# Optimization experiments

Hardware: AMD Instinct MI355X
Metric: run time of the kernel (lower is better)

Reference implementation:

```python
import jax, jax.numpy as jnp
import numpy as np

TAU = 5.0
ENTROPY_REG = 0.0  # entropy branch disabled (matches init kwargs)
NEG_INF = -1.0e9
NORM_EPS = 1e-12   # F.normalize eps
COS_EPS = 1e-8     # F.cosine_similarity eps


def _l2norm(x):
    n = jnp.sqrt(jnp.sum(x * x, axis=-1, keepdims=True))
    return x / jnp.maximum(n, NORM_EPS)


def setup_inputs() -> dict:
    key = jax.random.key(0)
    k1, k2, k3 = jax.random.split(key, 3)
    B, T, D = 8, 2048, 512
    pred_tokens = jax.random.normal(k1, (B, T, D), dtype=jnp.float32)
    text_tokens = jax.random.normal(k2, (B, T, D), dtype=jnp.float32)
    text_pad_mask = jax.random.randint(k3, (B, T), 0, 2).astype(jnp.bool_)  # True = PAD
    return {"pred_tokens": pred_tokens, "text_tokens": text_tokens, "text_pad_mask": text_pad_mask}


def reference(pred_tokens, text_tokens, text_pad_mask):
    B, Tp, D = pred_tokens.shape
    Tt = text_tokens.shape[1]
    T = min(Tp, Tt)
    P = _l2norm(pred_tokens[:, :T, :])            # [B,T,D]
    E = _l2norm(text_tokens[:, :T, :])            # [B,T,D]
    valid = ~text_pad_mask[:, :T]                 # [B,T] True = valid column

    S = jnp.einsum('btd,bsd->bts', P, E)          # [B,T,T]
    S = jnp.where(valid[:, None, :], S, NEG_INF)
    A = jax.nn.softmax(S * TAU, axis=-1)          # [B,T,T]
    E_hat = jnp.einsum('bts,bsd->btd', A, E)      # [B,T,D]

    # cosine similarity with eps-clamped norms (F.cosine_similarity semantics)
    dot = jnp.sum(P * E_hat, axis=-1)             # [B,T]
    pn = jnp.maximum(jnp.sqrt(jnp.sum(P * P, axis=-1)), COS_EPS)
    en = jnp.maximum(jnp.sqrt(jnp.sum(E_hat * E_hat, axis=-1)), COS_EPS)
    cos = dot / (pn * en)                         # [B,T]

    # row_has_valid: per-batch 'any valid column', broadcast over rows
    row_valid = jnp.broadcast_to(jnp.any(valid, axis=-1, keepdims=True), cos.shape)
    w = row_valid.astype(cos.dtype)
    cnt = jnp.sum(w)
    loss_sel = jnp.sum(w * (1.0 - cos)) / jnp.maximum(cnt, 1.0)
    loss = jnp.where(cnt > 0, loss_sel, jnp.zeros((), cos.dtype))
    tas = jnp.where(cnt > 0, 1.0 - jax.lax.stop_gradient(loss), loss)
    return (loss, tas)
```

## Files before the change

kernel.cpp:

```cpp
#include <hip/hip_runtime.h>
#include <cstdint>

typedef float f32x4 __attribute__((ext_vector_type(4)));
typedef long longx2 __attribute__((ext_vector_type(2)));
typedef unsigned char u8;
typedef unsigned short u16;
typedef unsigned int u32;
typedef unsigned long long u64;

#define B_N 8
#define T_N 2048
#define D_N 512
#define TAU 5.0f
#define NROW (B_N * T_N)
#define K1E 7.213475204444817f
#define K2E 1.4426950408889634f

#define WAITV(n) asm volatile("s_waitcnt vmcnt(" #n ")" ::: "memory")
#define BAR      __builtin_amdgcn_s_barrier()

__device__ __forceinline__ void gload_lds16(const u8* g, u8* l) {
  __builtin_amdgcn_global_load_lds(
      (const __attribute__((address_space(1))) u32*)g,
      (__attribute__((address_space(3))) u32*)l, 16, 0, 0);
}

__device__ __forceinline__ u32 pk4_fp8(float a, float b, float c, float d) {
  int w = __builtin_amdgcn_cvt_pk_fp8_f32(a, b, 0, 0);
  w = __builtin_amdgcn_cvt_pk_fp8_f32(c, d, w, 1);
  return (u32)w;
}

__device__ __forceinline__ u16 f2bf16(float x) {
  u32 u = __builtin_bit_cast(u32, x);
  u32 r = u + 0x7fffu + ((u >> 16) & 1u);
  return (u16)(r >> 16);
}
__device__ __forceinline__ float bf2f(u16 v) {
  u32 u = ((u32)v) << 16;
  return __builtin_bit_cast(float, u);
}

__global__ void kprep(const float* __restrict__ text,
                      u8* __restrict__ EF, u8* __restrict__ ET) {
  __shared__ u8 tile[32][528];
  int b = blockIdx.y, t = blockIdx.x;
  int tr = threadIdx.x;
  int row = tr >> 3, seg = tr & 7;
  const float* src = text + ((size_t)b * T_N + t * 32 + row) * D_N + seg * 64;
  float4 v[16];
  float ss = 0.f;
#pragma unroll
  for (int j = 0; j < 16; ++j) {
    v[j] = *(const float4*)(src + j * 4);
    ss += v[j].x*v[j].x + v[j].y*v[j].y + v[j].z*v[j].z + v[j].w*v[j].w;
  }
  ss += __shfl_xor(ss, 1); ss += __shfl_xor(ss, 2); ss += __shfl_xor(ss, 4);
  float inv = 1.f / fmaxf(sqrtf(ss), 1e-12f);
  u32 w[16];
#pragma unroll
  for (int j = 0; j < 16; ++j)
    w[j] = pk4_fp8(v[j].x*inv, v[j].y*inv, v[j].z*inv, v[j].w*inv);
  uint4* ldst = (uint4*)&tile[row][seg * 64];
#pragma unroll
  for (int j = 0; j < 4; ++j)
    ldst[j] = make_uint4(w[4*j], w[4*j+1], w[4*j+2], w[4*j+3]);
  __syncthreads();
  size_t tbase = ((size_t)(b * 64 + t)) << 14;
  {
    int j = tr >> 5, tok = tr & 31;
    u8* base = EF + tbase + j * 2048 + ((tok >> 4) << 10) + ((tok & 15) << 4);
#pragma unroll
    for (int g2 = 0; g2 < 4; ++g2) {
      uint2 h0 = *(const uint2*)&tile[tok][j*64 + g2*8];
      uint2 h1 = *(const uint2*)&tile[tok][j*64 + 32 + g2*8];
      *(uint4*)(base + g2 * 256) = make_uint4(h0.x, h0.y, h1.x, h1.y);
    }
  }
  {
    int m = tr >> 4, g2 = (tr >> 2) & 3, c0 = (tr & 3) * 4;
    u32 acc[16];
#pragma unroll
    for (int ci = 0; ci < 4; ++ci)
#pragma unroll
      for (int h = 0; h < 2; ++h) {
        int c = c0 + ci, n = 2*m + h;
        u32 lo = 0, hi = 0;
#pragma unroll
        for (int e = 0; e < 4; ++e) lo |= (u32)tile[g2*4 + e][n*16 + c] << (8*e);
#pragma unroll
        for (int e = 0; e < 4; ++e) hi |= (u32)tile[16 + g2*4 + e][n*16 + c] << (8*e);
        acc[ci*4 + h*2] = lo; acc[ci*4 + h*2 + 1] = hi;
      }
    uint4* dst = (uint4*)(ET + tbase + tr * 64);
#pragma unroll
    for (int q = 0; q < 4; ++q)
      dst[q] = make_uint4(acc[4*q], acc[4*q+1], acc[4*q+2], acc[4*q+3]);
  }
}

__launch_bounds__(512, 2)
__global__ void kflash(const float* __restrict__ pred,
                       const u8* __restrict__ EF, const u8* __restrict__ ET,
                       const int* __restrict__ mask,
                       u16* __restrict__ Opart, float* __restrict__ Lpart,
                       float* __restrict__ Dpart) {
  int b = blockIdx.x & 7;
  int rem = blockIdx.x >> 3;
  int rb = rem & 15, h = rem >> 4;
  int wid = threadIdx.x >> 6, lane = threadIdx.x & 63;
  int g = lane >> 4, c = lane & 15;
  int row0 = rb * 128 + wid * 16;
  int t0 = h * 32;
  const int l16 = lane << 4;

  __shared__ u64 mbits[32];
  __shared__ __align__(16) u8 els[2][16384];
  __shared__ __align__(16) u8 etls[2][16384];

  const u8* EFb = EF + (((size_t)(b * 64)) << 14) + l16;
  const u8* ETb = ET + (((size_t)(b * 64)) << 14) + l16;

  auto stageE = [&](int buf, int t) {
    size_t tb = ((size_t)t) << 14;
#pragma unroll
    for (int j = 0; j < 2; ++j) {
      int ch = wid * 2 + j;
      gload_lds16(EFb + tb + (ch << 10), &els[buf][ch << 10]);
    }
  };
  auto stageET = [&](int buf, int t) {
    size_t tb = ((size_t)t) << 14;
#pragma unroll
    for (int j = 0; j < 2; ++j) {
      int ch = wid * 2 + j;
      gload_lds16(ETb + tb + (ch << 10), &etls[buf][ch << 10]);
    }
  };

  for (int chunk = wid; chunk < 32; chunk += 8) {
    int col = chunk * 64 + lane;
    u64 bal = __ballot(mask[b * T_N + col] == 0);
    if (lane == 0) mbits[chunk] = bal;
  }

  stageE(0, t0); stageET(0, t0); stageE(1, t0 + 1);

  long pf[16];
  {
    int prow = row0 + c;
    const float* pr = pred + ((size_t)(b * T_N) + prow) * D_N;
    float ss = 0.f;
#pragma unroll
    for (int kk = 0; kk < 16; ++kk) {
      float4 v0 = *(const float4*)(pr + kk * 32 + g * 8);
      float4 v1 = *(const float4*)(pr + kk * 32 + g * 8 + 4);
      ss += v0.x*v0.x + v0.y*v0.y + v0.z*v0.z + v0.w*v0.w
          + v1.x*v1.x + v1.y*v1.y + v1.z*v1.z + v1.w*v1.w;
    }
    ss += __shfl_xor(ss, 16);
    ss += __shfl_xor(ss, 32);
    float inv = 1.f / fmaxf(sqrtf(ss), 1e-12f);
#pragma unroll
    for (int kk = 0; kk < 16; ++kk) {
      float4 v0 = *(const float4*)(pr + kk * 32 + g * 8);
      float4 v1 = *(const float4*)(pr + kk * 32 + g * 8 + 4);
      u32 lo = pk4_fp8(v0.x*inv, v0.y*inv, v0.z*inv, v0.w*inv);
      u32 hi = pk4_fp8(v1.x*inv, v1.y*inv, v1.z*inv, v1.w*inv);
      pf[kk] = (long)(((u64)hi << 32) | lo);
    }
  }

  __syncthreads();

  f32x4 zero = {0.f, 0.f, 0.f, 0.f};
  f32x4 eh[32];
#pragma unroll
  for (int n = 0; n < 32; ++n) eh[n] = zero;
  float lsum = 0.f, dsum = 0.f;

#pragma unroll 1
  for (int tt = 0; tt < 32; ++tt) {
    int cur = tt & 1;
    if (tt < 31) { WAITV(2); } else { WAITV(0); }
    BAR;

    if (tt < 31) stageET(cur ^ 1, t0 + tt + 1);
    const u8* el = &els[cur][0];
    longx2 rS0[2], rS1[2];
    rS0[0] = *(const longx2*)(el + l16);
    rS1[0] = *(const longx2*)(el + 1024 + l16);
    f32x4 a00 = zero, a01 = zero, a10 = zero, a11 = zero;
    __builtin_amdgcn_s_setprio(1);
#pragma unroll
    for (int j = 0; j < 8; ++j) {
      int pp = j & 1;
      if (j < 7) {
        rS0[pp ^ 1] = *(const longx2*)(el + (j + 1) * 2048 + l16);
        rS1[pp ^ 1] = *(const longx2*)(el + (j + 1) * 2048 + 1024 + l16);
      }
      a00 = __builtin_amdgcn_mfma_f32_16x16x32_fp8_fp8(rS0[pp][0], pf[2*j],   a00, 0, 0, 0);
      a01 = __builtin_amdgcn_mfma_f32_16x16x32_fp8_fp8(rS0[pp][1], pf[2*j+1], a01, 0, 0, 0);
      a10 = __builtin_amdgcn_mfma_f32_16x16x32_fp8_fp8(rS1[pp][0], pf[2*j],   a10, 0, 0, 0);
      a11 = __builtin_amdgcn_mfma_f32_16x16x32_fp8_fp8(rS1[pp][1], pf[2*j+1], a11, 0, 0, 0);
    }
    __builtin_amdgcn_s_setprio(0);
    f32x4 st0 = a00 + a01, st1 = a10 + a11;
    BAR;

    if (tt < 30) stageE(cur, t0 + tt + 2);
    int c0 = (t0 + tt) * 32;
    u64 mw = mbits[c0 >> 6];
    u32 sh0 = (c0 & 63) + g * 4;
    u32 bits0 = (u32)(mw >> sh0) & 0xf;
    u32 bits1 = (u32)(mw >> (sh0 + 16)) & 0xf;
    float p0[4], p1[4];
#pragma unroll
    for (int r = 0; r < 4; ++r) {
      p0[r] = (bits0 >> r) & 1 ? __builtin_exp2f(fmaf(K1E, st0[r], -K2E)) : 0.f;
      p1[r] = (bits1 >> r) & 1 ? __builtin_exp2f(fmaf(K1E, st1[r], -K2E)) : 0.f;
      lsum += p0[r] + p1[r];
      dsum += p0[r] * st0[r] + p1[r] * st1[r];
    }
    u32 lo = pk4_fp8(p0[0], p0[1], p0[2], p0[3]);
    u32 hi = pk4_fp8(p1[0], p1[1], p1[2], p1[3]);
    long af = (long)(((u64)hi << 32) | lo);

    const u8* et = &etls[cur][0];
    longx2 rV[2];
    rV[0] = *(const longx2*)(et + l16);
    __builtin_amdgcn_s_setprio(1);
#pragma unroll
    for (int m = 0; m < 16; ++m) {
      int pp = m & 1;
      if (m < 15) rV[pp ^ 1] = *(const longx2*)(et + (m + 1) * 1024 + l16);
      eh[2*m]   = __builtin_amdgcn_mfma_f32_16x16x32_fp8_fp8(af, rV[pp][0], eh[2*m],   0, 0, 0);
      eh[2*m+1] = __builtin_amdgcn_mfma_f32_16x16x32_fp8_fp8(af, rV[pp][1], eh[2*m+1], 0, 0, 0);
    }
    __builtin_amdgcn_s_setprio(0);
  }

  lsum += __shfl_xor(lsum, 16);
  lsum += __shfl_xor(lsum, 32);
  dsum += __shfl_xor(dsum, 16);
  dsum += __shfl_xor(dsum, 32);
  u16* OP = Opart + (size_t)h * ((size_t)NROW * D_N);
#pragma unroll
  for (int r = 0; r < 4; ++r) {
    int brow = b * T_N + row0 + g * 4 + r;
    u16* orow = OP + (size_t)brow * D_N + c;
#pragma unroll
    for (int n = 0; n < 32; ++n) orow[n * 16] = f2bf16(eh[n][r]);
  }
  if (g == 0) {
    Lpart[h * NROW + b * T_N + row0 + c] = lsum;
    Dpart[h * NROW + b * T_N + row0 + c] = dsum;
  }
}

__global__ void kcomb(const u16* __restrict__ Opart, const float* __restrict__ Lpart,
                      const float* __restrict__ Dpart,
                      float* __restrict__ pl, float* __restrict__ pw) {
  __shared__ float sl[8], swv[8];
  int tr = threadIdx.x;
  int row = blockIdx.x * 8 + (tr >> 5);
  int ln = tr & 31;
  float l = Lpart[row] + Lpart[NROW + row];
  float dot = Dpart[row] + Dpart[NROW + row];
  const u16* o0 = Opart + (size_t)row * D_N + ln * 16;
  const u16* o1 = o0 + (size_t)NROW * D_N;
  float e2 = 0.f;
#pragma unroll
  for (int q = 0; q < 2; ++q) {
    uint4 a0 = *(const uint4*)(o0 + q * 8);
    uint4 a1 = *(const uint4*)(o1 + q * 8);
    u32 w0[4] = {a0.x, a0.y, a0.z, a0.w};
    u32 w1[4] = {a1.x, a1.y, a1.z, a1.w};
#pragma unroll
    for (int j = 0; j < 8; ++j) {
      float f0 = bf2f((u16)((w0[j >> 1] >> ((j & 1) * 16)) & 0xffff));
      float f1 = bf2f((u16)((w1[j >> 1] >> ((j & 1) * 16)) & 0xffff));
      float ev = f0 + f1;
      e2 += ev * ev;
    }
  }
#pragma unroll
  for (int msk = 16; msk >= 1; msk >>= 1) e2 += __shfl_xor(e2, msk);
  if (ln == 0) {
    float w = (l > 0.f) ? 1.f : 0.f;
    float cosv = (l > 0.f) ? dot / fmaxf(sqrtf(e2), 1e-8f * l) : 0.f;
    sl[tr >> 5] = w * (1.f - cosv);
    swv[tr >> 5] = w;
  }
  __syncthreads();
  if (tr == 0) {
    float a = 0.f, b2 = 0.f;
#pragma unroll
    for (int i = 0; i < 8; ++i) { a += sl[i]; b2 += swv[i]; }
    pl[blockIdx.x] = a;
    pw[blockIdx.x] = b2;
  }
}

__global__ void kreduce(const float* __restrict__ pl, const float* __restrict__ pw,
                        float* __restrict__ out) {
  __shared__ float sm[256], sw[256];
  float s = 0.f, w = 0.f;
  for (int i = threadIdx.x; i < NROW / 8; i += 256) { s += pl[i]; w += pw[i]; }
  sm[threadIdx.x] = s; sw[threadIdx.x] = w;
  __syncthreads();
#pragma unroll
  for (int st = 128; st >= 1; st >>= 1) {
    if ((int)threadIdx.x < st) {
      sm[threadIdx.x] += sm[threadIdx.x + st];
      sw[threadIdx.x] += sw[threadIdx.x + st];
    }
    __syncthreads();
  }
  if (threadIdx.x == 0) {
    float cnt = sw[0];
    float loss = (cnt > 0.f) ? sm[0] / fmaxf(cnt, 1.f) : 0.f;
    out[0] = loss;
    out[1] = (cnt > 0.f) ? 1.f - loss : 0.f;
  }
}

extern "C" void kernel_launch(void* const* d_in, const int* in_sizes, int n_in,
                              void* d_out, int out_size, void* d_ws, size_t ws_size,
                              hipStream_t stream) {
  const float* pred = (const float*)d_in[0];
  const float* text = (const float*)d_in[1];
  const int* mask = (const int*)d_in[2];
  char* ws = (char*)d_ws;
  const size_t EB8 = (size_t)B_N * T_N * D_N;
  const size_t OB = (size_t)NROW * D_N * 2;
  u8* EF = (u8*)ws;
  u8* ET = (u8*)(ws + EB8);
  u16* Opart = (u16*)(ws + 2 * EB8);
  char* base2 = ws + 2 * EB8 + 2 * OB;
  float* Lpart = (float*)(base2);
  float* Dpart = (float*)(base2 + 131072);
  float* pl = (float*)(base2 + 262144);
  float* pw = (float*)(base2 + 262144 + 16384);
  float* out = (float*)d_out;

  kprep<<<dim3(64, 8), dim3(256), 0, stream>>>(text, EF, ET);
  kflash<<<dim3(256), dim3(512), 0, stream>>>(pred, EF, ET, mask, Opart, Lpart, Dpart);
  kcomb<<<dim3(NROW / 8), dim3(256), 0, stream>>>(Opart, Lpart, Dpart, pl, pw);
  kreduce<<<dim3(1), dim3(256), 0, stream>>>(pl, pw, out);
}
```

Baseline: 105.0 us.

## Fuse split-K combine into flash kernel via in-block LDS reduction

Each block now handles 64 rows, with its two halves of the key range (h=0/1) assigned to separate groups of four waves in the same block, instead of separate blocks writing bf16 partial outputs to global memory. The halves are combined through LDS: h=1 writes its accumulators to shared memory, h=0 sums them and computes the cosine loss per row. This removes the separate combine kernel and the global round-trip of partial outputs. In exchange, shared memory grows to about 130KB per block with launch bounds of one block per CU, which lowers occupancy, and each wave now stages more chunks per tile.

```diff
diff --git a/kernel.cpp b/kernel.cpp
--- a/kernel.cpp
+++ b/kernel.cpp
@@ -11,7 +11,6 @@
 #define B_N 8
 #define T_N 2048
 #define D_N 512
-#define TAU 5.0f
 #define NROW (B_N * T_N)
 #define K1E 7.213475204444817f
 #define K2E 1.4426950408889634f
@@ -99,24 +98,28 @@
   }
 }
 
-__launch_bounds__(512, 2)
+__launch_bounds__(512, 1)
 __global__ void kflash(const float* __restrict__ pred,
                        const u8* __restrict__ EF, const u8* __restrict__ ET,
                        const int* __restrict__ mask,
-                       u16* __restrict__ Opart, float* __restrict__ Lpart,
-                       float* __restrict__ Dpart) {
-  int b = blockIdx.x & 7;
-  int rem = blockIdx.x >> 3;
-  int rb = rem & 15, h = rem >> 4;
+                       float* __restrict__ pl, float* __restrict__ pw) {
+  int b = blockIdx.x & 7, rb = blockIdx.x >> 3;
   int wid = threadIdx.x >> 6, lane = threadIdx.x & 63;
   int g = lane >> 4, c = lane & 15;
-  int row0 = rb * 128 + wid * 16;
+  int h = wid >> 2, wg = wid & 3;
+  int row0 = rb * 64 + wg * 16;
   int t0 = h * 32;
   const int l16 = lane << 4;
 
-  __shared__ u64 mbits[32];
-  __shared__ __align__(16) u8 els[2][16384];
-  __shared__ __align__(16) u8 etls[2][16384];
+  __shared__ __align__(16) u8 smem[133120];
+  u8* els  = smem + h * 32768;
+  u8* etls = smem + 65536 + h * 32768;
+  u64* mbits = (u64*)(smem + 131072);
+  float* Lb = (float*)(smem + 131328);
+  float* Db = (float*)(smem + 131840);
+  float* slb = (float*)(smem + 132352);
+  float* swb = (float*)(smem + 132368);
+  u16* obuf = (u16*)smem;
 
   const u8* EFb = EF + (((size_t)(b * 64)) << 14) + l16;
   const u8* ETb = ET + (((size_t)(b * 64)) << 14) + l16;
@@ -124,17 +127,17 @@
   auto stageE = [&](int buf, int t) {
     size_t tb = ((size_t)t) << 14;
 #pragma unroll
-    for (int j = 0; j < 2; ++j) {
-      int ch = wid * 2 + j;
-      gload_lds16(EFb + tb + (ch << 10), &els[buf][ch << 10]);
+    for (int j = 0; j < 4; ++j) {
+      int ch = wg * 4 + j;
+      gload_lds16(EFb + tb + (ch << 10), els + buf * 16384 + (ch << 10));
     }
   };
   auto stageET = [&](int buf, int t) {
     size_t tb = ((size_t)t) << 14;
 #pragma unroll
-    for (int j = 0; j < 2; ++j) {
-      int ch = wid * 2 + j;
-      gload_lds16(ETb + tb + (ch << 10), &etls[buf][ch << 10]);
+    for (int j = 0; j < 4; ++j) {
+      int ch = wg * 4 + j;
+      gload_lds16(ETb + tb + (ch << 10), etls + buf * 16384 + (ch << 10));
     }
   };
 
@@ -182,11 +185,11 @@
 #pragma unroll 1
   for (int tt = 0; tt < 32; ++tt) {
     int cur = tt & 1;
-    if (tt < 31) { WAITV(2); } else { WAITV(0); }
+    if (tt < 31) { WAITV(4); } else { WAITV(0); }
     BAR;
 
     if (tt < 31) stageET(cur ^ 1, t0 + tt + 1);
-    const u8* el = &els[cur][0];
+    const u8* el = els + cur * 16384;
     longx2 rS0[2], rS1[2];
     rS0[0] = *(const longx2*)(el + l16);
     rS1[0] = *(const longx2*)(el + 1024 + l16);
@@ -226,7 +229,7 @@
     u32 hi = pk4_fp8(p1[0], p1[1], p1[2], p1[3]);
     long af = (long)(((u64)hi << 32) | lo);
 
-    const u8* et = &etls[cur][0];
+    const u8* et = etls + cur * 16384;
     longx2 rV[2];
     rV[0] = *(const longx2*)(et + l16);
     __builtin_amdgcn_s_setprio(1);
@@ -244,80 +247,77 @@
   lsum += __shfl_xor(lsum, 32);
   dsum += __shfl_xor(dsum, 16);
   dsum += __shfl_xor(dsum, 32);
-  u16* OP = Opart + (size_t)h * ((size_t)NROW * D_N);
-#pragma unroll
-  for (int r = 0; r < 4; ++r) {
-    int brow = b * T_N + row0 + g * 4 + r;
-    u16* orow = OP + (size_t)brow * D_N + c;
-#pragma unroll
-    for (int n = 0; n < 32; ++n) orow[n * 16] = f2bf16(eh[n][r]);
-  }
   if (g == 0) {
-    Lpart[h * NROW + b * T_N + row0 + c] = lsum;
-    Dpart[h * NROW + b * T_N + row0 + c] = dsum;
-  }
-}
-
-__global__ void kcomb(const u16* __restrict__ Opart, const float* __restrict__ Lpart,
-                      const float* __restrict__ Dpart,
-                      float* __restrict__ pl, float* __restrict__ pw) {
-  __shared__ float sl[8], swv[8];
-  int tr = threadIdx.x;
-  int row = blockIdx.x * 8 + (tr >> 5);
-  int ln = tr & 31;
-  float l = Lpart[row] + Lpart[NROW + row];
-  float dot = Dpart[row] + Dpart[NROW + row];
-  const u16* o0 = Opart + (size_t)row * D_N + ln * 16;
-  const u16* o1 = o0 + (size_t)NROW * D_N;
-  float e2 = 0.f;
-#pragma unroll
-  for (int q = 0; q < 2; ++q) {
-    uint4 a0 = *(const uint4*)(o0 + q * 8);
-    uint4 a1 = *(const uint4*)(o1 + q * 8);
-    u32 w0[4] = {a0.x, a0.y, a0.z, a0.w};
-    u32 w1[4] = {a1.x, a1.y, a1.z, a1.w};
-#pragma unroll
-    for (int j = 0; j < 8; ++j) {
-      float f0 = bf2f((u16)((w0[j >> 1] >> ((j & 1) * 16)) & 0xffff));
-      float f1 = bf2f((u16)((w1[j >> 1] >> ((j & 1) * 16)) & 0xffff));
-      float ev = f0 + f1;
-      e2 += ev * ev;
-    }
-  }
-#pragma unroll
-  for (int msk = 16; msk >= 1; msk >>= 1) e2 += __shfl_xor(e2, msk);
-  if (ln == 0) {
-    float w = (l > 0.f) ? 1.f : 0.f;
-    float cosv = (l > 0.f) ? dot / fmaxf(sqrtf(e2), 1e-8f * l) : 0.f;
-    sl[tr >> 5] = w * (1.f - cosv);
-    swv[tr >> 5] = w;
-  }
-  __syncthreads();
-  if (tr == 0) {
-    float a = 0.f, b2 = 0.f;
-#pragma unroll
-    for (int i = 0; i < 8; ++i) { a += sl[i]; b2 += swv[i]; }
-    pl[blockIdx.x] = a;
-    pw[blockIdx.x] = b2;
+    Lb[h * 64 + wg * 16 + c] = lsum;
+    Db[h * 64 + wg * 16 + c] = dsum;
+  }
+  __syncthreads();
+
+  if (h == 1) {
+#pragma unroll
+    for (int n = 0; n < 32; ++n) {
+      u32 lo2 = (u32)f2bf16(eh[n][0]) | ((u32)f2bf16(eh[n][1]) << 16);
+      u32 hi2 = (u32)f2bf16(eh[n][2]) | ((u32)f2bf16(eh[n][3]) << 16);
+      *(uint2*)&obuf[(n * 16 + c) * 68 + wg * 16 + g * 4] = make_uint2(lo2, hi2);
+    }
+  }
+  __syncthreads();
+
+  float cl = 0.f, wl = 0.f;
+  if (h == 0) {
+    float e2a[4] = {0.f, 0.f, 0.f, 0.f};
+#pragma unroll
+    for (int n = 0; n < 32; ++n) {
+      uint2 v = *(const uint2*)&obuf[(n * 16 + c) * 68 + wg * 16 + g * 4];
+      float s0 = eh[n][0] + bf2f((u16)(v.x & 0xffff));
+      float s1 = eh[n][1] + bf2f((u16)(v.x >> 16));
+      float s2 = eh[n][2] + bf2f((u16)(v.y & 0xffff));
+      float s3 = eh[n][3] + bf2f((u16)(v.y >> 16));
+      e2a[0] += s0 * s0; e2a[1] += s1 * s1;
+      e2a[2] += s2 * s2; e2a[3] += s3 * s3;
+    }
+#pragma unroll
+    for (int r = 0; r < 4; ++r) {
+      e2a[r] += __shfl_xor(e2a[r], 1);
+      e2a[r] += __shfl_xor(e2a[r], 2);
+      e2a[r] += __shfl_xor(e2a[r], 4);
+      e2a[r] += __shfl_xor(e2a[r], 8);
+    }
+    if (c == 0) {
+#pragma unroll
+      for (int r = 0; r < 4; ++r) {
+        int row = wg * 16 + g * 4 + r;
+        float l = Lb[row] + Lb[64 + row];
+        float dot = Db[row] + Db[64 + row];
+        float w = (l > 0.f) ? 1.f : 0.f;
+        float cosv = (l > 0.f) ? dot / fmaxf(sqrtf(e2a[r]), 1e-8f * l) : 0.f;
+        cl += w * (1.f - cosv);
+        wl += w;
+      }
+    }
+    cl += __shfl_xor(cl, 16); cl += __shfl_xor(cl, 32);
+    wl += __shfl_xor(wl, 16); wl += __shfl_xor(wl, 32);
+    if (lane == 0) { slb[wg] = cl; swb[wg] = wl; }
+  }
+  __syncthreads();
+  if (threadIdx.x == 0) {
+    pl[blockIdx.x] = slb[0] + slb[1] + slb[2] + slb[3];
+    pw[blockIdx.x] = swb[0] + swb[1] + swb[2] + swb[3];
   }
 }
 
 __global__ void kreduce(const float* __restrict__ pl, const float* __restrict__ pw,
                         float* __restrict__ out) {
   __shared__ float sm[256], sw[256];
-  float s = 0.f, w = 0.f;
-  for (int i = threadIdx.x; i < NROW / 8; i += 256) { s += pl[i]; w += pw[i]; }
-  sm[threadIdx.x] = s; sw[threadIdx.x] = w;
+  int t = threadIdx.x;
+  sm[t] = pl[t]; sw[t] = pw[t];
   __syncthreads();
 #pragma unroll
   for (int st = 128; st >= 1; st >>= 1) {
-    if ((int)threadIdx.x < st) {
-      sm[threadIdx.x] += sm[threadIdx.x + st];
-      sw[threadIdx.x] += sw[threadIdx.x + st];
-    }
+    if (t < st) { sm[t] += sm[t + st]; sw[t] += sw[t + st]; }
     __syncthreads();
   }
-  if (threadIdx.x == 0) {
+  if (t == 0) {
     float cnt = sw[0];
     float loss = (cnt > 0.f) ? sm[0] / fmaxf(cnt, 1.f) : 0.f;
     out[0] = loss;
@@ -333,19 +333,13 @@
   const int* mask = (const int*)d_in[2];
   char* ws = (char*)d_ws;
   const size_t EB8 = (size_t)B_N * T_N * D_N;
-  const size_t OB = (size_t)NROW * D_N * 2;
   u8* EF = (u8*)ws;
   u8* ET = (u8*)(ws + EB8);
-  u16* Opart = (u16*)(ws + 2 * EB8);
-  char* base2 = ws + 2 * EB8 + 2 * OB;
-  float* Lpart = (float*)(base2);
-  float* Dpart = (float*)(base2 + 131072);
-  float* pl = (float*)(base2 + 262144);
-  float* pw = (float*)(base2 + 262144 + 16384);
+  float* pl = (float*)(ws + 2 * EB8);
+  float* pw = (float*)(ws + 2 * EB8 + 4096);
   float* out = (float*)d_out;
 
   kprep<<<dim3(64, 8), dim3(256), 0, stream>>>(text, EF, ET);
-  kflash<<<dim3(256), dim3(512), 0, stream>>>(pred, EF, ET, mask, Opart, Lpart, Dpart);
-  kcomb<<<dim3(NROW / 8), dim3(256), 0, stream>>>(Opart, Lpart, Dpart, pl, pw);
+  kflash<<<dim3(256), dim3(512), 0, stream>>>(pred, EF, ET, mask, pl, pw);
   kreduce<<<dim3(1), dim3(256), 0, stream>>>(pl, pw, out);
 }
```

Result: faster. 93.76 us (-10.7%).
